# Kernel tuning notes

Hardware: AMD Instinct MI355X
Metric: run time of the kernel (lower is better)

## Reference

```python
import jax, jax.numpy as jnp
import numpy as np

BATCH = 32
IN_SHAPE = (64, 64)
OUT_SHAPE = (128, 128)


def setup_inputs() -> dict:
    key = jax.random.key(0)
    k1, k2 = jax.random.split(key)
    y = jax.random.normal(k1, (BATCH, *IN_SHAPE), dtype=jnp.float32)
    # normalized sample coordinates in [0,1), one per input dim
    xnew = jax.random.uniform(k2, (BATCH, *OUT_SHAPE, len(IN_SHAPE)), dtype=jnp.float32)
    return {"y": y, "xnew": xnew}


def reference(y, xnew):
    # y: [B, S1, S2]; xnew: [B, H, W, 2] with coords in [0,1)
    B = y.shape[0]
    s1, s2 = IN_SHAPE
    P = int(np.prod(OUT_SHAPE))
    x = xnew.reshape(B, P, 2)  # [B, P, 2]

    # FFT over spatial dims (dims 1..), as in torch.fft.fftn(..., dim=(1,2))
    F = jnp.fft.fftn(y, axes=(1, 2))  # [B, S1, S2] complex64

    # signed integer frequencies per dim (trigonometric interpolation)
    f1 = jnp.fft.fftfreq(s1).astype(jnp.float32) * s1  # [S1]
    f2 = jnp.fft.fftfreq(s2).astype(jnp.float32) * s2  # [S2]

    two_pi_i = 2j * jnp.pi
    # per-dim complex phase factors; separable NUFFT-type-2 evaluation
    E1 = jnp.exp(two_pi_i * x[..., 0:1] * f1)  # [B, P, S1]
    E2 = jnp.exp(two_pi_i * x[..., 1:2] * f2)  # [B, P, S2]

    # ynew[b,p] = (1/(S1*S2)) * sum_{k,m} F[b,k,m] E1[b,p,k] E2[b,p,m]
    ynew = jnp.einsum('bkm,bpk,bpm->bp', F, E1, E2) / (s1 * s2)
    ynew = jnp.real(ynew)
    return ynew.reshape(B, *OUT_SHAPE)
```

## Files before the change

### kernel.cpp

```cpp
#include <hip/hip_runtime.h>
#include <math.h>

typedef _Float16 f16x8 __attribute__((ext_vector_type(8)));
typedef _Float16 f16x2 __attribute__((ext_vector_type(2)));
typedef float    f32x4 __attribute__((ext_vector_type(4)));

union F16x8u { f16x8 v; f16x2 h[4]; };

__device__ __forceinline__ float cos1_hw(float x) { return __builtin_amdgcn_cosf(x); }
__device__ __forceinline__ float sin1_hw(float x) { return __builtin_amdgcn_sinf(x); }

__device__ __forceinline__ f16x2 pkrtz(float a, float b)
{
    return __builtin_bit_cast(f16x2, __builtin_amdgcn_cvt_pkrtz(a, b));
}


__global__ __launch_bounds__(256)
void dft_pass1(const float* __restrict__ y, f16x2* __restrict__ T)
{
    __shared__ float  YL[4096];
    __shared__ float2 tw[64];
    const int tid = threadIdx.x;
    const int b = blockIdx.x >> 3;
    const int g = blockIdx.x & 7;

    const float4* src = (const float4*)(y + (b << 12));
    float4* dst = (float4*)YL;
#pragma unroll
    for (int i = 0; i < 4; ++i) dst[tid + (i << 8)] = src[tid + (i << 8)];
    if (tid < 64) {
        const float a = (float)tid * (1.0f / 64.0f);
        tw[tid] = make_float2(cos1_hw(a), sin1_hw(a));
    }
    __syncthreads();

    const int k   = tid & 63;
    const int wv  = tid >> 6;
    const int n2a = (g << 3) + wv;
    const int n2b = n2a + 4;

    float Tr0 = 0.f, Ti0 = 0.f, Tr1 = 0.f, Ti1 = 0.f;
#pragma unroll 4
    for (int n1 = 0; n1 < 64; ++n1) {
        const float ya = YL[(n1 << 6) + n2a];
        const float yb = YL[(n1 << 6) + n2b];
        const float2 w = tw[(k * n1) & 63];
        Tr0 = fmaf(ya,  w.x, Tr0);
        Ti0 = fmaf(ya, -w.y, Ti0);
        Tr1 = fmaf(yb,  w.x, Tr1);
        Ti1 = fmaf(yb, -w.y, Ti1);
    }
    T[(b << 12) + (n2a << 6) + k] = pkrtz(Tr0, Ti0);
    T[(b << 12) + (n2b << 6) + k] = pkrtz(Tr1, Ti1);
}

__global__ __launch_bounds__(256)
void dft_pass2(const f16x2* __restrict__ T,
               _Float16* __restrict__ Frt, _Float16* __restrict__ Fit)
{
    __shared__ f16x2  TL[4096];
    __shared__ float2 tw[64];
    const int tid = threadIdx.x;
    const int b = blockIdx.x >> 3;
    const int g = blockIdx.x & 7;

    const float4* src = (const float4*)(T + (b << 12));
    float4* dst = (float4*)TL;
#pragma unroll
    for (int i = 0; i < 4; ++i) dst[tid + (i << 8)] = src[tid + (i << 8)];
    if (tid < 64) {
        const float a = (float)tid * (1.0f / 64.0f);
        tw[tid] = make_float2(cos1_hw(a), sin1_hw(a));
    }
    __syncthreads();

    const int k  = tid & 63;
    const int wv = tid >> 6;
    const int ma = (g << 3) + wv;
    const int mb = ma + 4;

    float Fr0 = 0.f, Fi0 = 0.f, Fr1 = 0.f, Fi1 = 0.f;
#pragma unroll 4
    for (int n2 = 0; n2 < 64; ++n2) {
        const f16x2 t = TL[(n2 << 6) + k];
        const float tr = (float)t[0];
        const float ti = (float)t[1];
        const float2 wa = tw[(ma * n2) & 63];
        const float2 wb = tw[(mb * n2) & 63];
        Fr0 = fmaf(tr, wa.x, Fr0); Fr0 = fmaf(ti,  wa.y, Fr0);
        Fi0 = fmaf(ti, wa.x, Fi0); Fi0 = fmaf(tr, -wa.y, Fi0);
        Fr1 = fmaf(tr, wb.x, Fr1); Fr1 = fmaf(ti,  wb.y, Fr1);
        Fi1 = fmaf(ti, wb.x, Fi1); Fi1 = fmaf(tr, -wb.y, Fi1);
    }
    const int oa = (b << 12) + (ma << 6) + k;
    const int ob = (b << 12) + (mb << 6) + k;
    Frt[oa] = (_Float16)Fr0;  Fit[oa] = (_Float16)Fi0;
    Frt[ob] = (_Float16)Fr1;  Fit[ob] = (_Float16)Fi1;
}

__global__ __launch_bounds__(1024, 4)
void fourier_interp_cplx(const _Float16* __restrict__ Frt,
                         const _Float16* __restrict__ Fit,
                         const float* __restrict__ xnew,
                         float* __restrict__ out)
{
    __shared__ float2 XY[2048];
    const int tid    = threadIdx.x;
    const int batch  = blockIdx.x >> 3;
    const int sgrp   = blockIdx.x & 7;
    const int pbase  = (batch << 14) + (sgrp << 11);

    XY[tid]        = ((const float2*)xnew)[pbase + tid];
    XY[tid + 1024] = ((const float2*)xnew)[pbase + tid + 1024];
    __syncthreads();

    const int lane = tid & 63;
    const int wv   = tid >> 6;
    const int quad = lane >> 4;
    const int lrow = lane & 15;

    const _Float16* Fr = Frt + (batch << 12);
    const _Float16* Fi = Fit + (batch << 12);
    f16x8 Ar[4][2], Ai[4][2];
#pragma unroll
    for (int nt = 0; nt < 4; ++nt)
#pragma unroll
        for (int kt = 0; kt < 2; ++kt) {
            const int off = (((nt << 4) + lrow) << 6) + (kt << 5) + (quad << 3);
            Ar[nt][kt] = *(const f16x8*)(Fr + off);
            Ai[nt][kt] = *(const f16x8*)(Fi + off);
        }

#pragma unroll 1
    for (int mt = 0; mt < 8; ++mt) {
        const int lpt = ((mt >> 1) << 9) + (wv << 5) + ((mt & 1) << 4);
        const float2 xv = XY[lpt + lrow];

        const float cs1 = cos1_hw(xv.x);
        const float sn1 = sin1_hw(xv.x);
        const float cs1b = fmaf(cs1, cs1, -(sn1 * sn1));
        const float sn1b = 2.0f * cs1 * sn1;

        f32x4 Gr[4], Gi[4];
#pragma unroll
        for (int nt = 0; nt < 4; ++nt) {
            Gr[nt] = (f32x4){0.f, 0.f, 0.f, 0.f};
            Gi[nt] = (f32x4){0.f, 0.f, 0.f, 0.f};
        }

#pragma unroll
        for (int kt = 0; kt < 2; ++kt) {
            const float fb = (float)((quad << 3) - (kt ? 32 : 0));
            float th = xv.x * fb;
            th -= floorf(th);
            float er0 = cos1_hw(th);
            float ei0 = sin1_hw(th);
            float er1 = fmaf(-ei0, sn1, er0 * cs1);
            float ei1 = fmaf( er0, sn1, ei0 * cs1);

            F16x8u ur, ui, un;
#pragma unroll
            for (int jp = 0; jp < 4; ++jp) {
                ur.h[jp] = pkrtz(er0, er1);
                ui.h[jp] = pkrtz(ei0, ei1);
                un.h[jp] = pkrtz(-ei0, -ei1);
                if (jp < 3) {
                    const float e0 = fmaf(-ei0, sn1b, er0 * cs1b);
                    ei0 = fmaf(er0, sn1b, ei0 * cs1b);
                    er0 = e0;
                    const float e1 = fmaf(-ei1, sn1b, er1 * cs1b);
                    ei1 = fmaf(er1, sn1b, ei1 * cs1b);
                    er1 = e1;
                }
            }
#pragma unroll
            for (int nt = 0; nt < 4; ++nt) {
                Gr[nt] = __builtin_amdgcn_mfma_f32_16x16x32_f16(Ar[nt][kt], ur.v, Gr[nt], 0, 0, 0);
                Gr[nt] = __builtin_amdgcn_mfma_f32_16x16x32_f16(Ai[nt][kt], un.v, Gr[nt], 0, 0, 0);
                Gi[nt] = __builtin_amdgcn_mfma_f32_16x16x32_f16(Ar[nt][kt], ui.v, Gi[nt], 0, 0, 0);
                Gi[nt] = __builtin_amdgcn_mfma_f32_16x16x32_f16(Ai[nt][kt], ur.v, Gi[nt], 0, 0, 0);
            }
        }

        const float cs2 = cos1_hw(xv.y);
        const float sn2 = sin1_hw(xv.y);
        float t16 = xv.y * 16.0f;
        t16 -= floorf(t16);
        const float c16 = cos1_hw(t16);
        const float s16 = sin1_hw(t16);
        const float cm32 = fmaf(c16, c16, -(s16 * s16));
        const float sm32 = -2.0f * c16 * s16;

        float thA = xv.y * (float)(quad << 2);
        thA -= floorf(thA);
        const float erA = cos1_hw(thA);
        const float eiA = sin1_hw(thA);

        float br[4], bi[4];
        br[0] = erA;                            bi[0] = eiA;
        br[1] = fmaf(-eiA, s16, erA * c16);     bi[1] = fmaf(erA, s16, eiA * c16);
        br[2] = fmaf(-eiA, sm32, erA * cm32);   bi[2] = fmaf(erA, sm32, eiA * cm32);
        br[3] = fmaf(-bi[2], s16, br[2] * c16); bi[3] = fmaf(br[2], s16, bi[2] * c16);

        float red = 0.0f;
#pragma unroll
        for (int nt = 0; nt < 4; ++nt) {
            float er = br[nt];
            float ei = bi[nt];
#pragma unroll
            for (int reg = 0; reg < 4; ++reg) {
                red = fmaf(Gr[nt][reg],  er, red);
                red = fmaf(Gi[nt][reg], -ei, red);
                if (reg < 3) {
                    const float t2 = fmaf(-ei, sn2, er * cs2);
                    ei = fmaf(er, sn2, ei * cs2);
                    er = t2;
                }
            }
        }
        red += __shfl_xor(red, 16, 64);
        red += __shfl_xor(red, 32, 64);
        if (lane < 16)
            out[pbase + lpt + lane] = red * (1.0f / 4096.0f);
    }
}

extern "C" void kernel_launch(void* const* d_in, const int* in_sizes, int n_in,
                              void* d_out, int out_size, void* d_ws, size_t ws_size,
                              hipStream_t stream)
{
    const float* y    = (const float*)d_in[0];
    const float* xnew = (const float*)d_in[1];
    float* out        = (float*)d_out;

    f16x2*    T   = (f16x2*)d_ws;
    _Float16* Frt = (_Float16*)((char*)d_ws + (32 << 14));
    _Float16* Fit = Frt + (32 << 12);

    dft_pass1<<<256, 256, 0, stream>>>(y, T);
    dft_pass2<<<256, 256, 0, stream>>>(T, Frt, Fit);
    fourier_interp_cplx<<<256, 1024, 0, stream>>>(Frt, Fit, xnew, out);
}
```

Before: 87.14 us.

## Fuse both DFT passes into the interpolation kernel via shared memory

Merges the two DFT kernels and the MFMA interpolation kernel into one launch. Each block recomputes its batch's 64x64 DFT in LDS, then loads the padded spectrum into registers. This removes two launches and the global workspace round trip. In exchange it adds 8x redundant DFT work per batch and raises LDS usage, which limits occupancy.

```diff
diff --git a/kernel.cpp b/kernel.cpp
--- a/kernel.cpp
+++ b/kernel.cpp
@@ -16,120 +16,78 @@
 }
 
 
-__global__ __launch_bounds__(256)
-void dft_pass1(const float* __restrict__ y, f16x2* __restrict__ T)
+__global__ __launch_bounds__(1024, 4)
+void fourier_fused(const float* __restrict__ y,
+                   const float* __restrict__ xnew,
+                   float* __restrict__ out)
 {
-    __shared__ float  YL[4096];
-    __shared__ float2 tw[64];
-    const int tid = threadIdx.x;
-    const int b = blockIdx.x >> 3;
-    const int g = blockIdx.x & 7;
+    __shared__ float    YL[4096];
+    __shared__ f16x2    TL[4096];
+    __shared__ _Float16 FrL[64 * 72];
+    __shared__ _Float16 FiL[64 * 72];
+    __shared__ float2   XY[2048];
+    __shared__ float2   tw[64];
 
-    const float4* src = (const float4*)(y + (b << 12));
-    float4* dst = (float4*)YL;
-#pragma unroll
-    for (int i = 0; i < 4; ++i) dst[tid + (i << 8)] = src[tid + (i << 8)];
+    const int tid   = threadIdx.x;
+    const int batch = blockIdx.x >> 3;
+    const int sgrp  = blockIdx.x & 7;
+    const int pbase = (batch << 14) + (sgrp << 11);
+
+    ((float4*)YL)[tid] = ((const float4*)(y + (batch << 12)))[tid];
+    ((float4*)XY)[tid] = ((const float4*)(xnew + ((size_t)pbase << 1)))[tid];
     if (tid < 64) {
         const float a = (float)tid * (1.0f / 64.0f);
         tw[tid] = make_float2(cos1_hw(a), sin1_hw(a));
     }
     __syncthreads();
 
-    const int k   = tid & 63;
-    const int wv  = tid >> 6;
-    const int n2a = (g << 3) + wv;
-    const int n2b = n2a + 4;
+    const int lane = tid & 63;
+    const int wv   = tid >> 6;
 
-    float Tr0 = 0.f, Ti0 = 0.f, Tr1 = 0.f, Ti1 = 0.f;
+#pragma unroll
+    for (int rep = 0; rep < 4; ++rep) {
+        const int n2 = wv + (rep << 4);
+        float Tr = 0.f, Ti = 0.f;
 #pragma unroll 4
-    for (int n1 = 0; n1 < 64; ++n1) {
-        const float ya = YL[(n1 << 6) + n2a];
-        const float yb = YL[(n1 << 6) + n2b];
-        const float2 w = tw[(k * n1) & 63];
-        Tr0 = fmaf(ya,  w.x, Tr0);
-        Ti0 = fmaf(ya, -w.y, Ti0);
-        Tr1 = fmaf(yb,  w.x, Tr1);
-        Ti1 = fmaf(yb, -w.y, Ti1);
-    }
-    T[(b << 12) + (n2a << 6) + k] = pkrtz(Tr0, Ti0);
-    T[(b << 12) + (n2b << 6) + k] = pkrtz(Tr1, Ti1);
-}
-
-__global__ __launch_bounds__(256)
-void dft_pass2(const f16x2* __restrict__ T,
-               _Float16* __restrict__ Frt, _Float16* __restrict__ Fit)
-{
-    __shared__ f16x2  TL[4096];
-    __shared__ float2 tw[64];
-    const int tid = threadIdx.x;
-    const int b = blockIdx.x >> 3;
-    const int g = blockIdx.x & 7;
-
-    const float4* src = (const float4*)(T + (b << 12));
-    float4* dst = (float4*)TL;
-#pragma unroll
-    for (int i = 0; i < 4; ++i) dst[tid + (i << 8)] = src[tid + (i << 8)];
-    if (tid < 64) {
-        const float a = (float)tid * (1.0f / 64.0f);
-        tw[tid] = make_float2(cos1_hw(a), sin1_hw(a));
+        for (int n1 = 0; n1 < 64; ++n1) {
+            const float yv = YL[(n1 << 6) + n2];
+            const float2 w = tw[(lane * n1) & 63];
+            Tr = fmaf(yv,  w.x, Tr);
+            Ti = fmaf(yv, -w.y, Ti);
+        }
+        TL[(n2 << 6) + lane] = pkrtz(Tr, Ti);
     }
     __syncthreads();
 
-    const int k  = tid & 63;
-    const int wv = tid >> 6;
-    const int ma = (g << 3) + wv;
-    const int mb = ma + 4;
-
-    float Fr0 = 0.f, Fi0 = 0.f, Fr1 = 0.f, Fi1 = 0.f;
+#pragma unroll
+    for (int rep = 0; rep < 4; ++rep) {
+        const int m = wv + (rep << 4);
+        float Fr = 0.f, Fi = 0.f;
 #pragma unroll 4
-    for (int n2 = 0; n2 < 64; ++n2) {
-        const f16x2 t = TL[(n2 << 6) + k];
-        const float tr = (float)t[0];
-        const float ti = (float)t[1];
-        const float2 wa = tw[(ma * n2) & 63];
-        const float2 wb = tw[(mb * n2) & 63];
-        Fr0 = fmaf(tr, wa.x, Fr0); Fr0 = fmaf(ti,  wa.y, Fr0);
-        Fi0 = fmaf(ti, wa.x, Fi0); Fi0 = fmaf(tr, -wa.y, Fi0);
-        Fr1 = fmaf(tr, wb.x, Fr1); Fr1 = fmaf(ti,  wb.y, Fr1);
-        Fi1 = fmaf(ti, wb.x, Fi1); Fi1 = fmaf(tr, -wb.y, Fi1);
+        for (int n2 = 0; n2 < 64; ++n2) {
+            const f16x2 t = TL[(n2 << 6) + lane];
+            const float tr = (float)t[0];
+            const float ti = (float)t[1];
+            const float2 w = tw[(m * n2) & 63];
+            Fr = fmaf(tr, w.x, Fr); Fr = fmaf(ti,  w.y, Fr);
+            Fi = fmaf(ti, w.x, Fi); Fi = fmaf(tr, -w.y, Fi);
+        }
+        FrL[m * 72 + lane] = (_Float16)Fr;
+        FiL[m * 72 + lane] = (_Float16)Fi;
     }
-    const int oa = (b << 12) + (ma << 6) + k;
-    const int ob = (b << 12) + (mb << 6) + k;
-    Frt[oa] = (_Float16)Fr0;  Fit[oa] = (_Float16)Fi0;
-    Frt[ob] = (_Float16)Fr1;  Fit[ob] = (_Float16)Fi1;
-}
-
-__global__ __launch_bounds__(1024, 4)
-void fourier_interp_cplx(const _Float16* __restrict__ Frt,
-                         const _Float16* __restrict__ Fit,
-                         const float* __restrict__ xnew,
-                         float* __restrict__ out)
-{
-    __shared__ float2 XY[2048];
-    const int tid    = threadIdx.x;
-    const int batch  = blockIdx.x >> 3;
-    const int sgrp   = blockIdx.x & 7;
-    const int pbase  = (batch << 14) + (sgrp << 11);
-
-    XY[tid]        = ((const float2*)xnew)[pbase + tid];
-    XY[tid + 1024] = ((const float2*)xnew)[pbase + tid + 1024];
     __syncthreads();
 
-    const int lane = tid & 63;
-    const int wv   = tid >> 6;
     const int quad = lane >> 4;
     const int lrow = lane & 15;
 
-    const _Float16* Fr = Frt + (batch << 12);
-    const _Float16* Fi = Fit + (batch << 12);
     f16x8 Ar[4][2], Ai[4][2];
 #pragma unroll
     for (int nt = 0; nt < 4; ++nt)
 #pragma unroll
         for (int kt = 0; kt < 2; ++kt) {
-            const int off = (((nt << 4) + lrow) << 6) + (kt << 5) + (quad << 3);
-            Ar[nt][kt] = *(const f16x8*)(Fr + off);
-            Ai[nt][kt] = *(const f16x8*)(Fi + off);
+            const int off = ((nt << 4) + lrow) * 72 + (kt << 5) + (quad << 3);
+            Ar[nt][kt] = *(const f16x8*)&FrL[off];
+            Ai[nt][kt] = *(const f16x8*)&FiL[off];
         }
 
 #pragma unroll 1
@@ -234,11 +192,5 @@
     const float* xnew = (const float*)d_in[1];
     float* out        = (float*)d_out;
 
-    f16x2*    T   = (f16x2*)d_ws;
-    _Float16* Frt = (_Float16*)((char*)d_ws + (32 << 14));
-    _Float16* Fit = Frt + (32 << 12);
-
-    dft_pass1<<<256, 256, 0, stream>>>(y, T);
-    dft_pass2<<<256, 256, 0, stream>>>(T, Frt, Fit);
-    fourier_interp_cplx<<<256, 1024, 0, stream>>>(Frt, Fit, xnew, out);
+    fourier_fused<<<256, 1024, 0, stream>>>(y, xnew, out);
 }
```

Result: slower. 99.51 us (+14.2%).
